# Performance work log

Hardware: AMD Instinct MI355X
Metric: run time of the kernel (lower is better)

Reference implementation:

```python
import jax, jax.numpy as jnp
import numpy as np
from jax import lax

N, D = 4096, 256
MAX_ITERS = 10
SHIFT_THRESHOLD = 1e-5
EPS = 1e-8


def _cosine_sim(a, b):
    # rows of a (M,D) vs rows of b (N,D) -> (M,N)
    an = a / jnp.clip(jnp.linalg.norm(a, axis=-1, keepdims=True), EPS)
    bn = b / jnp.clip(jnp.linalg.norm(b, axis=-1, keepdims=True), EPS)
    return an @ bn.T


def _mean_shift(x, sigma):
    inv_gamma = 1.0 / (2.0 * sigma ** 2)

    def step(carry, _):
        centroids, done = carry
        sim = _cosine_sim(centroids, x)                 # (N, N)
        weights = jnp.exp(2.0 * (sim - 1.0) * inv_gamma)
        new_c = (weights @ x) / jnp.sum(weights, axis=-1, keepdims=True)
        shift = jnp.max(jnp.linalg.norm(new_c - centroids, axis=-1))
        below = shift < SHIFT_THRESHOLD
        # torch breaks BEFORE assigning, so if below threshold keep old centroids
        centroids = jnp.where(done | below, centroids, new_c)
        return (centroids, done | below), None

    (centroids, _), _ = lax.scan(step, (x, jnp.array(False)), None, length=MAX_ITERS)
    return centroids


def _nms_mask(x, centroids, bandwidth):
    # Returns a boolean keep mask over the N centroids (jit-friendly analogue of
    # returning the unique kept indices).
    cp_dist = 2.0 * (1.0 - _cosine_sim(centroids, x))   # (M, N)
    p_to_closest_c = jnp.argmin(cp_dist, axis=0)        # (N,) closest centroid per point
    counts = jnp.zeros((centroids.shape[0],), dtype=jnp.float32).at[p_to_closest_c].add(1.0)
    cc_dist = 2.0 * (1.0 - _cosine_sim(centroids, centroids))
    cc_close = (cc_dist < bandwidth).astype(jnp.float32)
    # For every centroid row: index of the close centroid with the largest count.
    mapped = jnp.argmax(cc_close * counts[None, :], axis=1)   # (M,)
    valid = counts > 0                                        # rows in torch's closest_c
    keep = jnp.zeros((centroids.shape[0],), dtype=bool).at[mapped].max(valid)
    return keep


def setup_inputs() -> dict:
    key = jax.random.key(0)
    x = jax.random.normal(key, (N, D), dtype=jnp.float32)
    sigma = jnp.array(1.0, dtype=jnp.float32)
    return {"x": x, "sigma": sigma}


def reference(x, sigma):
    centroids = _mean_shift(x, sigma)
    keep = _nms_mask(x, centroids, sigma)
    # torch returns centroids[keep_idx] (data-dependent shape); for a jit-friendly
    # reference we return the full centroids plus the keep mask.
    return centroids, keep
```

## Files before the change

kernel.cpp:

```cpp
#include <hip/hip_runtime.h>
#include <math.h>

#define NPTS 4096
#define DIM  256
#define MAX_ITERS 10
#define EPSN 1e-8f
#define NSPL 16

typedef __bf16 bf16x8 __attribute__((ext_vector_type(8)));
typedef float  f32x4  __attribute__((ext_vector_type(4)));
typedef unsigned short u16x8 __attribute__((ext_vector_type(8)));
typedef unsigned short u16x4 __attribute__((ext_vector_type(4)));
typedef unsigned short U16;

__device__ __forceinline__ U16 bf16_rne(float f) {
    unsigned int u = __float_as_uint(f);
    u += 0x7FFFu + ((u >> 16) & 1u);
    return (U16)(u >> 16);
}

__device__ __forceinline__ void glds16(const void* g, void* l) {
    __builtin_amdgcn_global_load_lds(
        (const __attribute__((address_space(1))) unsigned int*)g,
        (__attribute__((address_space(3))) unsigned int*)l,
        16, 0, 0);
}

__global__ void initK(int* counts, int* keep, int* done, int* shiftb) {
    int i = blockIdx.x * 256 + threadIdx.x;
    if (i < NPTS) { counts[i] = 0; keep[i] = 0; }
    if (i == 0) { *done = 0; *shiftb = 0; }
}

__global__ void normxK(const float* __restrict__ x, float* __restrict__ c,
                       U16* __restrict__ xh, U16* __restrict__ xl) {
    int m = blockIdx.x, t = threadIdx.x;
    float v = x[(size_t)m*DIM + t];
    __shared__ float red[256];
    red[t] = v*v; __syncthreads();
    for (int s = 128; s > 0; s >>= 1) { if (t < s) red[t] += red[t+s]; __syncthreads(); }
    float rn = 1.0f / fmaxf(sqrtf(red[0]), EPSN);
    float hv = v*rn;
    U16 hb = bf16_rne(hv);
    float hf = __uint_as_float((unsigned)hb << 16);
    U16 lb = bf16_rne(hv - hf);
    c [(size_t)m*DIM + t] = v;
    xh[(size_t)m*DIM + t] = hb;
    xl[(size_t)m*DIM + t] = lb;
}

__global__ void transpK(const float* __restrict__ x, U16* __restrict__ Xth, U16* __restrict__ Xtl) {
    int bm = blockIdx.x, bd = blockIdx.y;
    int t = threadIdx.x;
    __shared__ float sh[32][33];
    int r = t >> 3, cq = (t & 7) * 4;
    float4 v = *(const float4*)&x[(size_t)(bm*32 + r)*DIM + bd*32 + cq];
    sh[r][cq] = v.x; sh[r][cq+1] = v.y; sh[r][cq+2] = v.z; sh[r][cq+3] = v.w;
    __syncthreads();
    int dd = t >> 3, mq = (t & 7) * 4;
    u16x4 h4, l4;
    #pragma unroll
    for (int j = 0; j < 4; ++j) {
        float f = sh[mq + j][dd];
        U16 hb = bf16_rne(f);
        h4[j] = hb;
        l4[j] = bf16_rne(f - __uint_as_float((unsigned)hb << 16));
    }
    size_t off = (size_t)(bd*32 + dd)*NPTS + bm*32 + mq;
    *(u16x4*)&Xth[off] = h4;
    *(u16x4*)&Xtl[off] = l4;
}

__global__ void normsplitK(float* __restrict__ c, const float* __restrict__ cnew,
                           U16* __restrict__ chh, U16* __restrict__ chl,
                           const int* __restrict__ done, int commit) {
    if (*done) return;
    int m = blockIdx.x, t = threadIdx.x;
    float v;
    if (commit) { v = cnew[(size_t)m*DIM + t]; c[(size_t)m*DIM + t] = v; }
    else        { v = c[(size_t)m*DIM + t]; }
    __shared__ float red[256];
    red[t] = v*v; __syncthreads();
    for (int s = 128; s > 0; s >>= 1) { if (t < s) red[t] += red[t+s]; __syncthreads(); }
    float rn = 1.0f / fmaxf(sqrtf(red[0]), EPSN);
    float hv = v*rn;
    U16 hb = bf16_rne(hv);
    float hf = __uint_as_float((unsigned)hb << 16);
    U16 lb = bf16_rne(hv - hf);
    chh[(size_t)m*DIM + t] = hb;
    chl[(size_t)m*DIM + t] = lb;
}

__global__ void normfinalK(const float* __restrict__ cen,
                           U16* __restrict__ hh, U16* __restrict__ ll) {
    int m = blockIdx.x, t = threadIdx.x;
    float v = cen[(size_t)m*DIM + t];
    __shared__ float red[256];
    red[t] = v*v; __syncthreads();
    for (int s = 128; s > 0; s >>= 1) { if (t < s) red[t] += red[t+s]; __syncthreads(); }
    float rn = 1.0f / fmaxf(sqrtf(red[0]), EPSN);
    float hv = v*rn;
    U16 hb = bf16_rne(hv);
    float hf = __uint_as_float((unsigned)hb << 16);
    U16 lb = bf16_rne(hv - hf);
    hh[(size_t)m*DIM + t] = hb;
    ll[(size_t)m*DIM + t] = lb;
}

#define WPAD 136
__global__ __launch_bounds__(256, 1) void fusedK(
    const U16* __restrict__ chh, const U16* __restrict__ chl,
    const U16* __restrict__ xh,  const U16* __restrict__ xl,
    const U16* __restrict__ xth, const U16* __restrict__ xtl,
    float* __restrict__ cnum, float* __restrict__ psum,
    const int* __restrict__ done, const float* __restrict__ sigma,
    int KLEN)
{
    if (*done) return;
    const int tid  = threadIdx.x;
    const int lane = tid & 63, wq = tid >> 6;
    const int l15  = lane & 15, lg = lane >> 4;
    const int slice = blockIdx.x;
    const int mblk  = blockIdx.y * 64;
    const int j0g  = slice * KLEN;

    __shared__ U16 WhL[64 * WPAD];
    __shared__ U16 WlL[64 * WPAD];
    __shared__ float psw[4][64];

    const float ig = 1.0f / (2.0f * (*sigma) * (*sigma));

    f32x4 acc2[4][4];
    #pragma unroll
    for (int a = 0; a < 4; ++a)
        #pragma unroll
        for (int b = 0; b < 4; ++b) { f32x4 z = {0.f,0.f,0.f,0.f}; acc2[a][b] = z; }
    float rs[4][4];
    #pragma unroll
    for (int a = 0; a < 4; ++a)
        #pragma unroll
        for (int i = 0; i < 4; ++i) rs[a][i] = 0.f;

    const int NJT = KLEN / 128;
    for (int jt = 0; jt < NJT; ++jt) {
        const int jb = j0g + jt * 128;

        f32x4 acc1[4][2];
        #pragma unroll
        for (int a = 0; a < 4; ++a)
            #pragma unroll
            for (int b = 0; b < 2; ++b) { f32x4 z = {0.f,0.f,0.f,0.f}; acc1[a][b] = z; }

        #pragma unroll
        for (int ks = 0; ks < 8; ++ks) {
            const int k0 = ks * 32 + lg * 8;
            bf16x8 ah[4], al[4], bh[2], bl[2];
            #pragma unroll
            for (int a = 0; a < 4; ++a) {
                size_t off = (size_t)(mblk + a*16 + l15)*DIM + k0;
                ah[a] = *(const bf16x8*)(chh + off);
                al[a] = *(const bf16x8*)(chl + off);
            }
            #pragma unroll
            for (int b = 0; b < 2; ++b) {
                size_t off = (size_t)(jb + wq*32 + b*16 + l15)*DIM + k0;
                bh[b] = *(const bf16x8*)(xh + off);
                bl[b] = *(const bf16x8*)(xl + off);
            }
            #pragma unroll
            for (int a = 0; a < 4; ++a)
                #pragma unroll
                for (int b = 0; b < 2; ++b) {
                    acc1[a][b] = __builtin_amdgcn_mfma_f32_16x16x32_bf16(ah[a], bh[b], acc1[a][b], 0,0,0);
                    acc1[a][b] = __builtin_amdgcn_mfma_f32_16x16x32_bf16(ah[a], bl[b], acc1[a][b], 0,0,0);
                    acc1[a][b] = __builtin_amdgcn_mfma_f32_16x16x32_bf16(al[a], bh[b], acc1[a][b], 0,0,0);
                }
        }

        __syncthreads();
        #pragma unroll
        for (int a = 0; a < 4; ++a)
            #pragma unroll
            for (int b = 0; b < 2; ++b)
                #pragma unroll
                for (int i = 0; i < 4; ++i) {
                    float w = __expf(2.0f * (acc1[a][b][i] - 1.0f) * ig);
                    U16 hb = bf16_rne(w);
                    float hf = __uint_as_float((unsigned)hb << 16);
                    U16 lb = bf16_rne(w - hf);
                    int m = a*16 + lg*4 + i;
                    int j = wq*32 + b*16 + l15;
                    WhL[m*WPAD + j] = hb;
                    WlL[m*WPAD + j] = lb;
                    rs[a][i] += w;
                }
        __syncthreads();

        #pragma unroll
        for (int ks = 0; ks < 4; ++ks) {
            bf16x8 wh[4], wl[4], xbh[4], xbl[4];
            const int jl = ks*32 + lg*8;
            #pragma unroll
            for (int a = 0; a < 4; ++a) {
                int m = a*16 + l15;
                wh[a] = *(const bf16x8*)&WhL[m*WPAD + jl];
                wl[a] = *(const bf16x8*)&WlL[m*WPAD + jl];
            }
            #pragma unroll
            for (int b = 0; b < 4; ++b) {
                size_t off = (size_t)(wq*64 + b*16 + l15)*NPTS + jb + jl;
                xbh[b] = *(const bf16x8*)(xth + off);
                xbl[b] = *(const bf16x8*)(xtl + off);
            }
            #pragma unroll
            for (int a = 0; a < 4; ++a)
                #pragma unroll
                for (int b = 0; b < 4; ++b) {
                    acc2[a][b] = __builtin_amdgcn_mfma_f32_16x16x32_bf16(wh[a], xbh[b], acc2[a][b], 0,0,0);
                    acc2[a][b] = __builtin_amdgcn_mfma_f32_16x16x32_bf16(wh[a], xbl[b], acc2[a][b], 0,0,0);
                    acc2[a][b] = __builtin_amdgcn_mfma_f32_16x16x32_bf16(wl[a], xbh[b], acc2[a][b], 0,0,0);
                }
        }
    }

    #pragma unroll
    for (int msk = 1; msk < 16; msk <<= 1)
        #pragma unroll
        for (int a = 0; a < 4; ++a)
            #pragma unroll
            for (int i = 0; i < 4; ++i)
                rs[a][i] += __shfl_xor(rs[a][i], msk, 64);
    if (l15 == 0) {
        #pragma unroll
        for (int a = 0; a < 4; ++a)
            #pragma unroll
            for (int i = 0; i < 4; ++i)
                psw[wq][a*16 + lg*4 + i] = rs[a][i];
    }
    __syncthreads();
    if (tid < 64)
        psum[(size_t)slice*NPTS + mblk + tid] =
            psw[0][tid] + psw[1][tid] + psw[2][tid] + psw[3][tid];

    #pragma unroll
    for (int a = 0; a < 4; ++a)
        #pragma unroll
        for (int b = 0; b < 4; ++b)
            #pragma unroll
            for (int i = 0; i < 4; ++i) {
                int m = mblk + a*16 + lg*4 + i;
                int d = wq*64 + b*16 + l15;
                cnum[((size_t)slice*NPTS + m)*DIM + d] = acc2[a][b][i];
            }
}

__global__ void reduceK(const float* __restrict__ psum, const float* __restrict__ cnum,
                        const float* __restrict__ c, float* __restrict__ cnew,
                        const int* __restrict__ done, int* __restrict__ shiftb, int spl)
{
    if (*done) return;
    int m = blockIdx.x, t = threadIdx.x;
    float rowsum = 0.f;
    for (int s = 0; s < spl; ++s) rowsum += psum[(size_t)s*NPTS + m];
    float num = 0.f;
    for (int s = 0; s < spl; ++s) num += cnum[((size_t)s*NPTS + m)*DIM + t];
    float cn = num / rowsum;
    cnew[(size_t)m*DIM + t] = cn;
    float d = cn - c[(size_t)m*DIM + t];
    __shared__ float red[256];
    red[t] = d*d; __syncthreads();
    for (int st = 128; st > 0; st >>= 1) { if (t < st) red[t] += red[t+st]; __syncthreads(); }
    if (t == 0) atomicMax(shiftb, __float_as_int(sqrtf(red[0])));
}

__global__ void flagK(int* done, int* shiftb) {
    float sh = __int_as_float(*shiftb);
    if (!*done && sh < 1e-5f) *done = 1;
    *shiftb = 0;
}

__global__ void finalK(const int* __restrict__ done, const float* __restrict__ c,
                       const float* __restrict__ cnew, float* __restrict__ out) {
    int i = blockIdx.x*256 + threadIdx.x;
    out[i] = (*done) ? c[i] : cnew[i];
}

__global__ __launch_bounds__(256) void argminMK(
    const U16* __restrict__ Ph, const U16* __restrict__ Pl,
    const U16* __restrict__ Ch, const U16* __restrict__ Cl,
    float* __restrict__ aval, int* __restrict__ aidx)
{
    const int tid = threadIdx.x;
    const int lane = tid & 63, wid = tid >> 6;
    const int wr = wid & 1, wc = wid >> 1;
    const int P  = blockIdx.x * 128;
    const int ms = blockIdx.y;
    const int M0 = ms * (NPTS / NSPL);

    __shared__ U16 S[4][4096];
    __shared__ float fmv[128][2];
    __shared__ int   fmi[128][2];

    float pv[16];
    int   pm[16];
    #pragma unroll
    for (int s = 0; s < 16; ++s) { pv[s] = 3.4e38f; pm[s] = 0; }

    for (int mt = 0; mt < (NPTS/NSPL)/128; ++mt) {
        const int M = M0 + mt*128;
        f32x4 acc[4][4];
        #pragma unroll
        for (int a = 0; a < 4; ++a)
            #pragma unroll
            for (int b = 0; b < 4; ++b) { f32x4 z = {0.f,0.f,0.f,0.f}; acc[a][b] = z; }

        for (int k0 = 0; k0 < DIM; k0 += 32) {
            __syncthreads();
            #pragma unroll
            for (int h = 0; h < 2; ++h) {
                const int sb   = wid * 128 + h * 64;
                const int slot = sb + lane;
                const int row  = slot & 127, kg = slot >> 7;
                const int col  = k0 + kg * 8;
                glds16(Ph + (size_t)(P + row)*DIM + col, &S[0][(size_t)sb * 8]);
                glds16(Pl + (size_t)(P + row)*DIM + col, &S[1][(size_t)sb * 8]);
                glds16(Ch + (size_t)(M + row)*DIM + col, &S[2][(size_t)sb * 8]);
                glds16(Cl + (size_t)(M + row)*DIM + col, &S[3][(size_t)sb * 8]);
            }
            __syncthreads();
            bf16x8 fah[4], fal[4], fbh[4], fbl[4];
            const int roff = (lane >> 4) * 128 + (lane & 15);
            #pragma unroll
            for (int f = 0; f < 4; ++f) {
                const int sA = roff + wr*64 + f*16;
                const int sB = roff + wc*64 + f*16;
                fah[f] = *(const bf16x8*)&S[0][(size_t)sA * 8];
                fal[f] = *(const bf16x8*)&S[1][(size_t)sA * 8];
                fbh[f] = *(const bf16x8*)&S[2][(size_t)sB * 8];
                fbl[f] = *(const bf16x8*)&S[3][(size_t)sB * 8];
            }
            #pragma unroll
            for (int a = 0; a < 4; ++a)
                #pragma unroll
                for (int b = 0; b < 4; ++b) {
                    acc[a][b] = __builtin_amdgcn_mfma_f32_16x16x32_bf16(fah[a], fbh[b], acc[a][b], 0,0,0);
                    acc[a][b] = __builtin_amdgcn_mfma_f32_16x16x32_bf16(fah[a], fbl[b], acc[a][b], 0,0,0);
                    acc[a][b] = __builtin_amdgcn_mfma_f32_16x16x32_bf16(fal[a], fbh[b], acc[a][b], 0,0,0);
                }
        }
        #pragma unroll
        for (int a = 0; a < 4; ++a)
            #pragma unroll
            for (int i = 0; i < 4; ++i) {
                const int s = a*4 + i;
                #pragma unroll
                for (int b = 0; b < 4; ++b) {
                    float d = 2.0f*(1.0f - acc[a][b][i]);
                    int m = M + wc*64 + b*16 + (lane & 15);
                    if (d < pv[s] || (d == pv[s] && m < pm[s])) { pv[s]=d; pm[s]=m; }
                }
            }
    }
    #pragma unroll
    for (int msk = 1; msk < 16; msk <<= 1)
        #pragma unroll
        for (int s = 0; s < 16; ++s) {
            float v2 = __shfl_xor(pv[s], msk, 64);
            int   m2 = __shfl_xor(pm[s], msk, 64);
            if (v2 < pv[s] || (v2 == pv[s] && m2 < pm[s])) { pv[s]=v2; pm[s]=m2; }
        }
    if ((lane & 15) == 0) {
        #pragma unroll
        for (int a = 0; a < 4; ++a)
            #pragma unroll
            for (int i = 0; i < 4; ++i) {
                int row = wr*64 + a*16 + (lane>>4)*4 + i;
                fmv[row][wc] = pv[a*4+i];
                fmi[row][wc] = pm[a*4+i];
            }
    }
    __syncthreads();
    if (tid < 128) {
        float v = fmv[tid][0]; int m = fmi[tid][0];
        float v1 = fmv[tid][1]; int m1 = fmi[tid][1];
        if (v1 < v || (v1 == v && m1 < m)) { v=v1; m=m1; }
        aval[(size_t)ms*NPTS + P + tid] = v;
        aidx[(size_t)ms*NPTS + P + tid] = m;
    }
}

__global__ void acombineK(const float* __restrict__ aval, const int* __restrict__ aidx,
                          int* __restrict__ counts)
{
    int p = blockIdx.x*256 + threadIdx.x;
    float bv = 3.4e38f; int bm = 1<<30;
    for (int s = 0; s < NSPL; ++s) {
        float v = aval[(size_t)s*NPTS + p]; int m = aidx[(size_t)s*NPTS + p];
        if (v < bv || (v == bv && m < bm)) { bv=v; bm=m; }
    }
    atomicAdd(&counts[bm], 1);
}

__global__ __launch_bounds__(256) void ccMK(
    const U16* __restrict__ Ch, const U16* __restrict__ Cl,
    const int* __restrict__ counts, const float* __restrict__ sigma,
    float* __restrict__ cval, int* __restrict__ cidx)
{
    const int tid = threadIdx.x;
    const int lane = tid & 63, wid = tid >> 6;
    const int wr = wid & 1, wc = wid >> 1;
    const int Mrow = blockIdx.x * 128;
    const int js   = blockIdx.y;
    const int J0   = js * (NPTS / NSPL);
    const float bw = *sigma;

    __shared__ U16 S[4][4096];
    __shared__ float gmv[128][2];
    __shared__ int   gmi[128][2];
    __shared__ float scnt[128];

    float mvv[16];
    int   mjj[16];
    #pragma unroll
    for (int s = 0; s < 16; ++s) { mvv[s] = -1.f; mjj[s] = 1<<30; }

    for (int jt = 0; jt < (NPTS/NSPL)/128; ++jt) {
        const int J = J0 + jt*128;
        __syncthreads();
        if (tid < 128) scnt[tid] = (float)counts[J + tid];
        f32x4 acc[4][4];
        #pragma unroll
        for (int a = 0; a < 4; ++a)
            #pragma unroll
            for (int b = 0; b < 4; ++b) { f32x4 z = {0.f,0.f,0.f,0.f}; acc[a][b] = z; }

        for (int k0 = 0; k0 < DIM; k0 += 32) {
            __syncthreads();
            #pragma unroll
            for (int h = 0; h < 2; ++h) {
                const int sb   = wid * 128 + h * 64;
                const int slot = sb + lane;
                const int row  = slot & 127, kg = slot >> 7;
                const int col  = k0 + kg * 8;
                glds16(Ch + (size_t)(Mrow + row)*DIM + col, &S[0][(size_t)sb * 8]);
                glds16(Cl + (size_t)(Mrow + row)*DIM + col, &S[1][(size_t)sb * 8]);
                glds16(Ch + (size_t)(J + row)*DIM + col,    &S[2][(size_t)sb * 8]);
                glds16(Cl + (size_t)(J + row)*DIM + col,    &S[3][(size_t)sb * 8]);
            }
            __syncthreads();
            bf16x8 fah[4], fal[4], fbh[4], fbl[4];
            const int roff = (lane >> 4) * 128 + (lane & 15);
            #pragma unroll
            for (int f = 0; f < 4; ++f) {
                const int sA = roff + wr*64 + f*16;
                const int sB = roff + wc*64 + f*16;
                fah[f] = *(const bf16x8*)&S[0][(size_t)sA * 8];
                fal[f] = *(const bf16x8*)&S[1][(size_t)sA * 8];
                fbh[f] = *(const bf16x8*)&S[2][(size_t)sB * 8];
                fbl[f] = *(const bf16x8*)&S[3][(size_t)sB * 8];
            }
            #pragma unroll
            for (int a = 0; a < 4; ++a)
                #pragma unroll
                for (int b = 0; b < 4; ++b) {
                    acc[a][b] = __builtin_amdgcn_mfma_f32_16x16x32_bf16(fah[a], fbh[b], acc[a][b], 0,0,0);
                    acc[a][b] = __builtin_amdgcn_mfma_f32_16x16x32_bf16(fah[a], fbl[b], acc[a][b], 0,0,0);
                    acc[a][b] = __builtin_amdgcn_mfma_f32_16x16x32_bf16(fal[a], fbh[b], acc[a][b], 0,0,0);
                }
        }
        #pragma unroll
        for (int a = 0; a < 4; ++a)
            #pragma unroll
            for (int i = 0; i < 4; ++i) {
                const int s = a*4 + i;
                #pragma unroll
                for (int b = 0; b < 4; ++b) {
                    float d = 2.0f*(1.0f - acc[a][b][i]);
                    int jl = wc*64 + b*16 + (lane & 15);
                    float val = (d < bw) ? scnt[jl] : 0.0f;
                    int j = J + jl;
                    if (val > mvv[s] || (val == mvv[s] && j < mjj[s])) { mvv[s]=val; mjj[s]=j; }
                }
            }
    }
    #pragma unroll
    for (int msk = 1; msk < 16; msk <<= 1)
        #pragma unroll
        for (int s = 0; s < 16; ++s) {
            float v2 = __shfl_xor(mvv[s], msk, 64);
            int   j2 = __shfl_xor(mjj[s], msk, 64);
            if (v2 > mvv[s] || (v2 == mvv[s] && j2 < mjj[s])) { mvv[s]=v2; mjj[s]=j2; }
        }
    if ((lane & 15) == 0) {
        #pragma unroll
        for (int a = 0; a < 4; ++a)
            #pragma unroll
            for (int i = 0; i < 4; ++i) {
                int row = wr*64 + a*16 + (lane>>4)*4 + i;
                gmv[row][wc] = mvv[a*4+i];
                gmi[row][wc] = mjj[a*4+i];
            }
    }
    __syncthreads();
    if (tid < 128) {
        float v = gmv[tid][0]; int j = gmi[tid][0];
        float v1 = gmv[tid][1]; int j1 = gmi[tid][1];
        if (v1 > v || (v1 == v && j1 < j)) { v=v1; j=j1; }
        cval[(size_t)js*NPTS + Mrow + tid] = v;
        cidx[(size_t)js*NPTS + Mrow + tid] = j;
    }
}

__global__ void ccombineK(const float* __restrict__ cval, const int* __restrict__ cidx,
                          const int* __restrict__ counts, int* __restrict__ keep)
{
    int m = blockIdx.x*256 + threadIdx.x;
    float bv = -1.0f; int bj = 1<<30;
    for (int s = 0; s < NSPL; ++s) {
        float v = cval[(size_t)s*NPTS + m]; int j = cidx[(size_t)s*NPTS + m];
        if (v > bv || (v == bv && j < bj)) { bv=v; bj=j; }
    }
    if (counts[m] > 0) atomicOr(&keep[bj], 1);
}

__global__ void keepwriteK(const int* __restrict__ keep, float* __restrict__ out)
{
    int i = blockIdx.x*256 + threadIdx.x;
    out[(size_t)NPTS*DIM + i] = keep[i] ? 1.0f : 0.0f;
}

extern "C" void kernel_launch(void* const* d_in, const int* in_sizes, int n_in,
                              void* d_out, int out_size, void* d_ws, size_t ws_size,
                              hipStream_t stream)
{
    const float* x     = (const float*)d_in[0];
    const float* sigma = (const float*)d_in[1];
    float* out = (float*)d_out;

    const size_t ND4 = (size_t)NPTS * DIM * 4;
    const size_t NDu = (size_t)NPTS * DIM * 2;

    const int spls[] = {4, 2, 1};
    int SPL = 1;
    size_t o_xh=0,o_xl=0,o_xth=0,o_xtl=0,o_chh=0,o_chl=0,o_c=0,o_cn=0,
           o_cnum=0,o_psum=0,o_aval=0,o_aidx=0,o_cval=0,o_cidx=0,
           o_counts=0,o_keep=0,o_done=0,o_shift=0;

    for (int ci = 0; ci < 3; ++ci) {
        int spl = spls[ci];
        size_t off = 0;
        auto take = [&](size_t nb) { size_t a = off; off += (nb + 255) & ~(size_t)255; return a; };
        o_xh  = take(NDu);  o_xl  = take(NDu);
        o_xth = take(NDu);  o_xtl = take(NDu);
        o_chh = take(NDu);  o_chl = take(NDu);
        o_c   = take(ND4);  o_cn  = take(ND4);
        o_cnum = take((size_t)spl * ND4);
        o_psum = take((size_t)spl * NPTS * 4);
        o_aval = take((size_t)NSPL*NPTS*4); o_aidx = take((size_t)NSPL*NPTS*4);
        o_cval = take((size_t)NSPL*NPTS*4); o_cidx = take((size_t)NSPL*NPTS*4);
        o_counts = take((size_t)NPTS*4);    o_keep = take((size_t)NPTS*4);
        o_done = take(256); o_shift = take(256);
        SPL = spl;
        if (off <= ws_size) break;
    }
    const int KLEN = NPTS / SPL;

    char* W = (char*)d_ws;
    U16* xh  = (U16*)(W + o_xh);   U16* xl  = (U16*)(W + o_xl);
    U16* xth = (U16*)(W + o_xth);  U16* xtl = (U16*)(W + o_xtl);
    U16* chh = (U16*)(W + o_chh);  U16* chl = (U16*)(W + o_chl);
    float* c    = (float*)(W + o_c);
    float* cnew = (float*)(W + o_cn);
    float* cnum = (float*)(W + o_cnum);
    float* psum = (float*)(W + o_psum);
    float* aval = (float*)(W + o_aval); int* aidx = (int*)(W + o_aidx);
    float* cval = (float*)(W + o_cval); int* cidx = (int*)(W + o_cidx);
    int* counts = (int*)(W + o_counts); int* keep = (int*)(W + o_keep);
    int* done   = (int*)(W + o_done);   int* shiftb = (int*)(W + o_shift);

    initK  <<<dim3(16), dim3(256), 0, stream>>>(counts, keep, done, shiftb);
    normxK <<<dim3(NPTS), dim3(256), 0, stream>>>(x, c, xh, xl);
    transpK<<<dim3(128, 8), dim3(256), 0, stream>>>(x, xth, xtl);

    for (int it = 0; it < MAX_ITERS; ++it) {
        normsplitK<<<dim3(NPTS), dim3(256), 0, stream>>>(c, cnew, chh, chl, done, it > 0);
        fusedK<<<dim3(SPL, NPTS/64), dim3(256), 0, stream>>>(
            chh, chl, xh, xl, xth, xtl, cnum, psum, done, sigma, KLEN);
        reduceK<<<dim3(NPTS), dim3(256), 0, stream>>>(psum, cnum, c, cnew, done, shiftb, SPL);
        flagK  <<<dim3(1), dim3(1), 0, stream>>>(done, shiftb);
    }

    finalK    <<<dim3(NPTS), dim3(256), 0, stream>>>(done, c, cnew, out);
    normfinalK<<<dim3(NPTS), dim3(256), 0, stream>>>(out, chh, chl);

    argminMK<<<dim3(NPTS/128, NSPL), dim3(256), 0, stream>>>(xh, xl, chh, chl, aval, aidx);
    acombineK<<<dim3(NPTS/256), dim3(256), 0, stream>>>(aval, aidx, counts);
    ccMK    <<<dim3(NPTS/128, NSPL), dim3(256), 0, stream>>>(chh, chl, counts, sigma, cval, cidx);
    ccombineK<<<dim3(NPTS/256), dim3(256), 0, stream>>>(cval, cidx, counts, keep);
    keepwriteK<<<dim3(NPTS/256), dim3(256), 0, stream>>>(keep, out);
}
```

Baseline: 1.689 ms.

## Fuse centroid normalization into reduce and rotate centroid buffers

Removes the per-iteration normsplitK launch by computing the normalized bf16 hi/lo split of the new centroids inside reduceK. Three rotating centroid buffers plus an index of the last accepted buffer replace the copy-on-commit step. The first iteration reads the precomputed normalized x directly. The split-count candidates also grow from {4,2,1} to {8,4,2}, giving more k-slices in fusedK at the cost of larger partial buffers and more reduction work.

```diff
diff --git a/kernel.cpp b/kernel.cpp
--- a/kernel.cpp
+++ b/kernel.cpp
@@ -26,13 +26,13 @@
         16, 0, 0);
 }
 
-__global__ void initK(int* counts, int* keep, int* done, int* shiftb) {
+__global__ void initK(int* counts, int* keep, int* done, int* shiftb, int* acc) {
     int i = blockIdx.x * 256 + threadIdx.x;
     if (i < NPTS) { counts[i] = 0; keep[i] = 0; }
-    if (i == 0) { *done = 0; *shiftb = 0; }
-}
-
-__global__ void normxK(const float* __restrict__ x, float* __restrict__ c,
+    if (i == 0) { *done = 0; *shiftb = 0; *acc = 0; }
+}
+
+__global__ void normxK(const float* __restrict__ x, float* __restrict__ c0,
                        U16* __restrict__ xh, U16* __restrict__ xl) {
     int m = blockIdx.x, t = threadIdx.x;
     float v = x[(size_t)m*DIM + t];
@@ -44,7 +44,7 @@
     U16 hb = bf16_rne(hv);
     float hf = __uint_as_float((unsigned)hb << 16);
     U16 lb = bf16_rne(hv - hf);
-    c [(size_t)m*DIM + t] = v;
+    c0[(size_t)m*DIM + t] = v;
     xh[(size_t)m*DIM + t] = hb;
     xl[(size_t)m*DIM + t] = lb;
 }
@@ -69,42 +69,6 @@
     size_t off = (size_t)(bd*32 + dd)*NPTS + bm*32 + mq;
     *(u16x4*)&Xth[off] = h4;
     *(u16x4*)&Xtl[off] = l4;
-}
-
-__global__ void normsplitK(float* __restrict__ c, const float* __restrict__ cnew,
-                           U16* __restrict__ chh, U16* __restrict__ chl,
-                           const int* __restrict__ done, int commit) {
-    if (*done) return;
-    int m = blockIdx.x, t = threadIdx.x;
-    float v;
-    if (commit) { v = cnew[(size_t)m*DIM + t]; c[(size_t)m*DIM + t] = v; }
-    else        { v = c[(size_t)m*DIM + t]; }
-    __shared__ float red[256];
-    red[t] = v*v; __syncthreads();
-    for (int s = 128; s > 0; s >>= 1) { if (t < s) red[t] += red[t+s]; __syncthreads(); }
-    float rn = 1.0f / fmaxf(sqrtf(red[0]), EPSN);
-    float hv = v*rn;
-    U16 hb = bf16_rne(hv);
-    float hf = __uint_as_float((unsigned)hb << 16);
-    U16 lb = bf16_rne(hv - hf);
-    chh[(size_t)m*DIM + t] = hb;
-    chl[(size_t)m*DIM + t] = lb;
-}
-
-__global__ void normfinalK(const float* __restrict__ cen,
-                           U16* __restrict__ hh, U16* __restrict__ ll) {
-    int m = blockIdx.x, t = threadIdx.x;
-    float v = cen[(size_t)m*DIM + t];
-    __shared__ float red[256];
-    red[t] = v*v; __syncthreads();
-    for (int s = 128; s > 0; s >>= 1) { if (t < s) red[t] += red[t+s]; __syncthreads(); }
-    float rn = 1.0f / fmaxf(sqrtf(red[0]), EPSN);
-    float hv = v*rn;
-    U16 hb = bf16_rne(hv);
-    float hf = __uint_as_float((unsigned)hb << 16);
-    U16 lb = bf16_rne(hv - hf);
-    hh[(size_t)m*DIM + t] = hb;
-    ll[(size_t)m*DIM + t] = lb;
 }
 
 #define WPAD 136
@@ -255,7 +219,8 @@
 }
 
 __global__ void reduceK(const float* __restrict__ psum, const float* __restrict__ cnum,
-                        const float* __restrict__ c, float* __restrict__ cnew,
+                        const float* __restrict__ cprev, float* __restrict__ ccur,
+                        U16* __restrict__ chh, U16* __restrict__ chl,
                         const int* __restrict__ done, int* __restrict__ shiftb, int spl)
 {
     if (*done) return;
@@ -265,24 +230,58 @@
     float num = 0.f;
     for (int s = 0; s < spl; ++s) num += cnum[((size_t)s*NPTS + m)*DIM + t];
     float cn = num / rowsum;
-    cnew[(size_t)m*DIM + t] = cn;
-    float d = cn - c[(size_t)m*DIM + t];
+    ccur[(size_t)m*DIM + t] = cn;
+    float d = cn - cprev[(size_t)m*DIM + t];
+    __shared__ float redd[256], redn[256];
+    redd[t] = d*d; redn[t] = cn*cn;
+    __syncthreads();
+    for (int st = 128; st > 0; st >>= 1) {
+        if (t < st) { redd[t] += redd[t+st]; redn[t] += redn[t+st]; }
+        __syncthreads();
+    }
+    if (t == 0) atomicMax(shiftb, __float_as_int(sqrtf(redd[0])));
+    float rn = 1.0f / fmaxf(sqrtf(redn[0]), EPSN);
+    float hv = cn * rn;
+    U16 hb = bf16_rne(hv);
+    float hf = __uint_as_float((unsigned)hb << 16);
+    U16 lb = bf16_rne(hv - hf);
+    chh[(size_t)m*DIM + t] = hb;
+    chl[(size_t)m*DIM + t] = lb;
+}
+
+__global__ void flagK(int* done, int* shiftb, int* acc, int curidx) {
+    if (!*done) {
+        float sh = __int_as_float(*shiftb);
+        if (sh < 1e-5f) *done = 1;
+        else *acc = curidx;
+    }
+    *shiftb = 0;
+}
+
+__global__ void finalK(const float* __restrict__ p0, const float* __restrict__ p1,
+                       const float* __restrict__ p2, const int* __restrict__ acc,
+                       float* __restrict__ out) {
+    int i = blockIdx.x*256 + threadIdx.x;
+    const float* p = (*acc == 0) ? p0 : ((*acc == 1) ? p1 : p2);
+    out[i] = p[i];
+}
+
+__global__ void normfinalK(const float* __restrict__ p0, const float* __restrict__ p1,
+                           const float* __restrict__ p2, const int* __restrict__ acc,
+                           U16* __restrict__ hh, U16* __restrict__ ll) {
+    int m = blockIdx.x, t = threadIdx.x;
+    const float* p = (*acc == 0) ? p0 : ((*acc == 1) ? p1 : p2);
+    float v = p[(size_t)m*DIM + t];
     __shared__ float red[256];
-    red[t] = d*d; __syncthreads();
-    for (int st = 128; st > 0; st >>= 1) { if (t < st) red[t] += red[t+st]; __syncthreads(); }
-    if (t == 0) atomicMax(shiftb, __float_as_int(sqrtf(red[0])));
-}
-
-__global__ void flagK(int* done, int* shiftb) {
-    float sh = __int_as_float(*shiftb);
-    if (!*done && sh < 1e-5f) *done = 1;
-    *shiftb = 0;
-}
-
-__global__ void finalK(const int* __restrict__ done, const float* __restrict__ c,
-                       const float* __restrict__ cnew, float* __restrict__ out) {
-    int i = blockIdx.x*256 + threadIdx.x;
-    out[i] = (*done) ? c[i] : cnew[i];
+    red[t] = v*v; __syncthreads();
+    for (int s = 128; s > 0; s >>= 1) { if (t < s) red[t] += red[t+s]; __syncthreads(); }
+    float rn = 1.0f / fmaxf(sqrtf(red[0]), EPSN);
+    float hv = v*rn;
+    U16 hb = bf16_rne(hv);
+    float hf = __uint_as_float((unsigned)hb << 16);
+    U16 lb = bf16_rne(hv - hf);
+    hh[(size_t)m*DIM + t] = hb;
+    ll[(size_t)m*DIM + t] = lb;
 }
 
 __global__ __launch_bounds__(256) void argminMK(
@@ -540,11 +539,11 @@
     const size_t ND4 = (size_t)NPTS * DIM * 4;
     const size_t NDu = (size_t)NPTS * DIM * 2;
 
-    const int spls[] = {4, 2, 1};
-    int SPL = 1;
-    size_t o_xh=0,o_xl=0,o_xth=0,o_xtl=0,o_chh=0,o_chl=0,o_c=0,o_cn=0,
+    const int spls[] = {8, 4, 2};
+    int SPL = 2;
+    size_t o_xh=0,o_xl=0,o_xth=0,o_xtl=0,o_chh=0,o_chl=0,o_c0=0,o_c1=0,o_c2=0,
            o_cnum=0,o_psum=0,o_aval=0,o_aidx=0,o_cval=0,o_cidx=0,
-           o_counts=0,o_keep=0,o_done=0,o_shift=0;
+           o_counts=0,o_keep=0,o_done=0,o_shift=0,o_acc=0;
 
     for (int ci = 0; ci < 3; ++ci) {
         int spl = spls[ci];
@@ -553,13 +552,13 @@
         o_xh  = take(NDu);  o_xl  = take(NDu);
         o_xth = take(NDu);  o_xtl = take(NDu);
         o_chh = take(NDu);  o_chl = take(NDu);
-        o_c   = take(ND4);  o_cn  = take(ND4);
+        o_c0  = take(ND4);  o_c1  = take(ND4);  o_c2 = take(ND4);
         o_cnum = take((size_t)spl * ND4);
         o_psum = take((size_t)spl * NPTS * 4);
         o_aval = take((size_t)NSPL*NPTS*4); o_aidx = take((size_t)NSPL*NPTS*4);
         o_cval = take((size_t)NSPL*NPTS*4); o_cidx = take((size_t)NSPL*NPTS*4);
         o_counts = take((size_t)NPTS*4);    o_keep = take((size_t)NPTS*4);
-        o_done = take(256); o_shift = take(256);
+        o_done = take(256); o_shift = take(256); o_acc = take(256);
         SPL = spl;
         if (off <= ws_size) break;
     }
@@ -569,29 +568,33 @@
     U16* xh  = (U16*)(W + o_xh);   U16* xl  = (U16*)(W + o_xl);
     U16* xth = (U16*)(W + o_xth);  U16* xtl = (U16*)(W + o_xtl);
     U16* chh = (U16*)(W + o_chh);  U16* chl = (U16*)(W + o_chl);
-    float* c    = (float*)(W + o_c);
-    float* cnew = (float*)(W + o_cn);
+    float* cb[3] = { (float*)(W + o_c0), (float*)(W + o_c1), (float*)(W + o_c2) };
     float* cnum = (float*)(W + o_cnum);
     float* psum = (float*)(W + o_psum);
     float* aval = (float*)(W + o_aval); int* aidx = (int*)(W + o_aidx);
     float* cval = (float*)(W + o_cval); int* cidx = (int*)(W + o_cidx);
     int* counts = (int*)(W + o_counts); int* keep = (int*)(W + o_keep);
     int* done   = (int*)(W + o_done);   int* shiftb = (int*)(W + o_shift);
-
-    initK  <<<dim3(16), dim3(256), 0, stream>>>(counts, keep, done, shiftb);
-    normxK <<<dim3(NPTS), dim3(256), 0, stream>>>(x, c, xh, xl);
+    int* acc    = (int*)(W + o_acc);
+
+    initK  <<<dim3(16), dim3(256), 0, stream>>>(counts, keep, done, shiftb, acc);
+    normxK <<<dim3(NPTS), dim3(256), 0, stream>>>(x, cb[0], xh, xl);
     transpK<<<dim3(128, 8), dim3(256), 0, stream>>>(x, xth, xtl);
 
     for (int it = 0; it < MAX_ITERS; ++it) {
-        normsplitK<<<dim3(NPTS), dim3(256), 0, stream>>>(c, cnew, chh, chl, done, it > 0);
+        const U16* ah = (it == 0) ? xh : chh;
+        const U16* al = (it == 0) ? xl : chl;
+        const int cur = 1 + (it & 1);
+        const int prv = (it == 0) ? 0 : 1 + ((it - 1) & 1);
         fusedK<<<dim3(SPL, NPTS/64), dim3(256), 0, stream>>>(
-            chh, chl, xh, xl, xth, xtl, cnum, psum, done, sigma, KLEN);
-        reduceK<<<dim3(NPTS), dim3(256), 0, stream>>>(psum, cnum, c, cnew, done, shiftb, SPL);
-        flagK  <<<dim3(1), dim3(1), 0, stream>>>(done, shiftb);
-    }
-
-    finalK    <<<dim3(NPTS), dim3(256), 0, stream>>>(done, c, cnew, out);
-    normfinalK<<<dim3(NPTS), dim3(256), 0, stream>>>(out, chh, chl);
+            ah, al, xh, xl, xth, xtl, cnum, psum, done, sigma, KLEN);
+        reduceK<<<dim3(NPTS), dim3(256), 0, stream>>>(
+            psum, cnum, cb[prv], cb[cur], chh, chl, done, shiftb, SPL);
+        flagK<<<dim3(1), dim3(1), 0, stream>>>(done, shiftb, acc, cur);
+    }
+
+    finalK    <<<dim3(NPTS), dim3(256), 0, stream>>>(cb[0], cb[1], cb[2], acc, out);
+    normfinalK<<<dim3(NPTS), dim3(256), 0, stream>>>(cb[0], cb[1], cb[2], acc, chh, chl);
 
     argminMK<<<dim3(NPTS/128, NSPL), dim3(256), 0, stream>>>(xh, xl, chh, chl, aval, aidx);
     acombineK<<<dim3(NPTS/256), dim3(256), 0, stream>>>(aval, aidx, counts);
```

Result: slower. 1.765 ms (+4.4%).
